# Kernel optimization log

Hardware: AMD Instinct MI355X
Metric: run time of the kernel (lower is better)

## Reference

```python
import jax, jax.numpy as jnp
import numpy as np

N_CLUSTERS = 2048
MAX_ITER = 5


def setup_inputs() -> dict:
    key = jax.random.key(0)
    k1, k2 = jax.random.split(key)
    X = jax.random.normal(k1, (131072, 128), dtype=jnp.float32)
    init_centroids = jax.random.normal(k2, (N_CLUSTERS, 128), dtype=jnp.float32)
    return {"X": X, "init_centroids": init_centroids}


def _euc_sim(a, b):
    # 2 a.b^T - |a|^2 - |b|^2  (negative squared euclidean distance)
    return (2.0 * (a @ b.T)
            - jnp.sum(a * a, axis=1)[:, None]
            - jnp.sum(b * b, axis=1)[None, :])


def reference(X, init_centroids):
    K = init_centroids.shape[0]

    def step(centroids, _):
        sim = _euc_sim(X, centroids)              # [N, K]
        closest = jnp.argmax(sim, axis=-1)         # [N]
        sums = jax.ops.segment_sum(X, closest, num_segments=K)        # [K, d]
        counts = jax.ops.segment_sum(jnp.ones_like(closest, dtype=X.dtype),
                                     closest, num_segments=K)         # [K]
        # full-batch branch: c_grad = mask @ x / mask.sum(-1), NaN -> 0
        c_grad = jnp.where(counts[:, None] > 0, sums / jnp.maximum(counts, 1.0)[:, None], 0.0)
        # minibatch is None => lr = 1 => centroids <- c_grad
        return c_grad, closest

    centroids, closest_hist = jax.lax.scan(step, init_centroids, None, length=MAX_ITER)
    labels = closest_hist[-1]
    return centroids, labels
```

## Files before the change

### kernel.cpp

```cpp
#include <hip/hip_runtime.h>
#include <hip/hip_bf16.h>

#define NP 131072
#define D 128
#define KC 2048
#define ITERS 5
#define CG 8

#define TAU 0.015f
#define CNOFF 49152

#if defined(__has_builtin)
#if __has_builtin(__builtin_amdgcn_global_load_lds)
#define USE_GLL 1
#endif
#endif

typedef short bf16x8 __attribute__((ext_vector_type(8)));
typedef float f32x4 __attribute__((ext_vector_type(4)));

__device__ inline unsigned short f2bf(float x) {
    __hip_bfloat16 b = __float2bfloat16(x);
    return *reinterpret_cast<unsigned short*>(&b);
}
__device__ inline float bf2f(unsigned short u) {
    union { unsigned int i; float f; } c; c.i = ((unsigned int)u) << 16; return c.f;
}

__device__ inline size_t pslot(int k, int d, int hl) {
    int g = k >> 4, t15 = k & 15, ks = d >> 5, q = (d >> 3) & 3, e = d & 7;
    return ((size_t)((ks * 128 + g) * 2 + hl)) * 512 + (q * 16 + t15) * 8 + e;
}

#if USE_GLL
#define GLL16(srcp, dstp) __builtin_amdgcn_global_load_lds( \
    (const __attribute__((address_space(1))) unsigned int*)(srcp), \
    (__attribute__((address_space(3))) unsigned int*)(dstp), 16, 0, 0)
#define GLL4(srcp, dstp) __builtin_amdgcn_global_load_lds( \
    (const __attribute__((address_space(1))) unsigned int*)(srcp), \
    (__attribute__((address_space(3))) unsigned int*)(dstp), 4, 0, 0)
#else
#define GLL16(srcp, dstp) do { *(uint4*)((char*)(dstp) + lane * 16) = *(const uint4*)(srcp); } while (0)
#define GLL4(srcp, dstp)  do { *(unsigned int*)((char*)(dstp) + lane * 4) = *(const unsigned int*)(srcp); } while (0)
#endif

__global__ void init_kernel(const float* __restrict__ initC,
                            double* __restrict__ C64, double* __restrict__ CT64,
                            unsigned short* __restrict__ Pn,
                            double* __restrict__ cn64, float* __restrict__ cn32,
                            int* __restrict__ counter) {
    __shared__ double sred[4];
    int tid = threadIdx.x;
    int t = blockIdx.x * 256 + tid;
    float v = initC[t];
    double dv = (double)v;
    C64[t] = dv;
    CT64[(size_t)(t & 127) * KC + (t >> 7)] = dv;
    unsigned short h = f2bf(v);
    int k = t >> 7, d = t & 127;
    Pn[pslot(k, d, 0)] = h;
    Pn[pslot(k, d, 1)] = f2bf(v - bf2f(h));
    double s = dv * dv;
#pragma unroll
    for (int m = 1; m < 64; m <<= 1) s += __shfl_xor(s, m, 64);
    if ((tid & 63) == 0) sred[tid >> 6] = s;
    __syncthreads();
    if (tid == 0)   { double ss = sred[0] + sred[1]; cn64[k] = ss; cn32[k] = (float)ss; }
    if (tid == 128) { double ss = sred[2] + sred[3]; cn64[k] = ss; cn32[k] = (float)ss; }
    if (blockIdx.x == 0 && tid == 0) *counter = 0;
}

__global__ __launch_bounds__(256, 3)
void assign_kernel(const float* __restrict__ X,
                   const unsigned short* __restrict__ Pn,
                   const float* __restrict__ cnorm,
                   int* __restrict__ labels,
                   int* __restrict__ list,
                   int* __restrict__ counter) {
    __shared__ __align__(16) char lds[49664];

    const int tid = threadIdx.x;
    const int lane = tid & 63;
    const int wid = tid >> 6;
    const int wrow = wid >> 1;
    const int wcol = wid & 1;
    const int t15 = lane & 15;
    const int q = lane >> 4;
    const int pbase = blockIdx.x * 64;
    const char* PnB = (const char*)Pn;

#pragma unroll
    for (int i = 0; i < 8; i++) {
        int f = i * 256 + tid;
        int row = f >> 5, c4 = f & 31;
        float4 v = *(const float4*)&X[(size_t)(pbase + row) * D + c4 * 4];
        unsigned short h0 = f2bf(v.x), h1 = f2bf(v.y), h2 = f2bf(v.z), h3 = f2bf(v.w);
        unsigned short l0 = f2bf(v.x - bf2f(h0)), l1 = f2bf(v.y - bf2f(h1));
        unsigned short l2 = f2bf(v.z - bf2f(h2)), l3 = f2bf(v.w - bf2f(h3));
        uint2 ph = { (unsigned)h0 | ((unsigned)h1 << 16), (unsigned)h2 | ((unsigned)h3 << 16) };
        uint2 pl = { (unsigned)l0 | ((unsigned)l1 << 16), (unsigned)l2 | ((unsigned)l3 << 16) };
        int ad = (row * 256 + c4 * 8) ^ ((row & 7) << 4);
        *(uint2*)(lds + ad) = ph;
        *(uint2*)(lds + 16384 + ad) = pl;
    }
    __syncthreads();

    bf16x8 rah[2][4], ral[2][4];
#pragma unroll
    for (int rt = 0; rt < 2; rt++) {
        int row = wrow * 32 + rt * 16 + t15;
        int sw = (row & 7) << 4;
#pragma unroll
        for (int ks = 0; ks < 4; ks++) {
            int ad = (row * 256 + ks * 64 + q * 16) ^ sw;
            rah[rt][ks] = *(const bf16x8*)(lds + ad);
            ral[rt][ks] = *(const bf16x8*)(lds + 16384 + ad);
        }
    }
    __syncthreads();

    float b1[8], b2[8];
    int i1[8];
#pragma unroll
    for (int s = 0; s < 8; s++) { b1[s] = -INFINITY; b2[s] = -INFINITY; i1[s] = 0x7fffffff; }

#pragma unroll
    for (int i = 0; i < 4; i++) {
        int seg = wid * 4 + i;
        GLL16(PnB + seg * 1024 + lane * 16, lds + seg * 1024);
    }
#pragma unroll
    for (int i = 0; i < 4; i++) {
        int seg = wid * 4 + i;
        GLL16(PnB + (size_t)(1 * 128) * 2048 + seg * 1024 + lane * 16,
              lds + 16384 + seg * 1024);
    }

#define STEP(KS, VMSTR) do {                                                  \
        asm volatile("s_waitcnt vmcnt(" VMSTR ")" ::: "memory");              \
        __builtin_amdgcn_s_barrier();                                         \
        asm volatile("" ::: "memory");                                        \
        __builtin_amdgcn_sched_barrier(0);                                    \
        int t_ = ct * 4 + (KS);                                               \
        int s2_ = t_ + 2;                                                     \
        int s2c_ = (s2_ > 63) ? 63 : s2_;                                     \
        char* bstage_ = lds + (unsigned)(s2_ % 3) * 16384;                    \
        const char* nsrc_ = PnB + ((size_t)((s2c_ & 3) * 128 + (s2c_ >> 2) * 8)) * 2048; \
        _Pragma("unroll")                                                     \
        for (int i_ = 0; i_ < 4; i_++) {                                      \
            int seg_ = wid * 4 + i_;                                          \
            GLL16(nsrc_ + seg_ * 1024 + lane * 16, bstage_ + seg_ * 1024);    \
        }                                                                     \
        if ((KS) == 0) {                                                      \
            const float* cs_ = cnorm + ct * 128;                              \
            GLL4(cs_ + lane, lds + CNOFF);                                    \
            GLL4(cs_ + 64 + lane, lds + CNOFF + 256);                         \
        }                                                                     \
        const char* bcur_ = lds + (unsigned)(t_ % 3) * 16384;                 \
        __builtin_amdgcn_s_setprio(1);                                        \
        _Pragma("unroll")                                                     \
        for (int cj_ = 0; cj_ < 4; cj_++) {                                   \
            int gl_ = wcol * 4 + cj_;                                         \
            bf16x8 bh_ = *(const bf16x8*)(bcur_ + gl_ * 2048 + lane * 16);    \
            bf16x8 bl_ = *(const bf16x8*)(bcur_ + gl_ * 2048 + 1024 + lane * 16); \
            _Pragma("unroll")                                                 \
            for (int rt_ = 0; rt_ < 2; rt_++) {                               \
                acc[rt_][cj_] = __builtin_amdgcn_mfma_f32_16x16x32_bf16(rah[rt_][KS], bh_, acc[rt_][cj_], 0, 0, 0); \
                acc[rt_][cj_] = __builtin_amdgcn_mfma_f32_16x16x32_bf16(rah[rt_][KS], bl_, acc[rt_][cj_], 0, 0, 0); \
                acc[rt_][cj_] = __builtin_amdgcn_mfma_f32_16x16x32_bf16(ral[rt_][KS], bh_, acc[rt_][cj_], 0, 0, 0); \
            }                                                                 \
        }                                                                     \
        __builtin_amdgcn_s_setprio(0);                                        \
    } while (0)

    for (int ct = 0; ct < KC / 128; ct++) {
        f32x4 acc[2][4];
#pragma unroll
        for (int rt = 0; rt < 2; rt++)
#pragma unroll
            for (int cj = 0; cj < 4; cj++) acc[rt][cj] = (f32x4){0.f, 0.f, 0.f, 0.f};

        STEP(0, "4");
        STEP(1, "6");
        STEP(2, "6");
        STEP(3, "4");

        const float* cnL = (const float*)(lds + CNOFF);
#pragma unroll
        for (int cj = 0; cj < 4; cj++) {
            int col = ct * 128 + wcol * 64 + cj * 16 + t15;
            float cnv = cnL[wcol * 64 + cj * 16 + t15];
#pragma unroll
            for (int rt = 0; rt < 2; rt++)
#pragma unroll
                for (int rg = 0; rg < 4; rg++) {
                    int s = rt * 4 + rg;
                    float sv = __builtin_fmaf(2.0f, acc[rt][cj][rg], -cnv);
                    float nb2 = __builtin_amdgcn_fmed3f(b1[s], b2[s], sv);
                    bool gt1 = sv > b1[s];
                    i1[s] = gt1 ? col : i1[s];
                    b1[s] = fmaxf(b1[s], sv);
                    b2[s] = nb2;
                }
        }
    }
#undef STEP

#pragma unroll
    for (int s = 0; s < 8; s++) {
#pragma unroll
        for (int m = 1; m < 16; m <<= 1) {
            float ob1 = __shfl_xor(b1[s], m, 64);
            int   oi  = __shfl_xor(i1[s], m, 64);
            float ob2 = __shfl_xor(b2[s], m, 64);
            bool gt = ob1 > b1[s];
            bool eq = ob1 == b1[s];
            float nb2 = gt ? fmaxf(b1[s], ob2) : fmaxf(b2[s], ob1);
            nb2 = eq ? b1[s] : nb2;
            int ni = gt ? oi : i1[s];
            ni = (eq && oi < i1[s]) ? oi : ni;
            b1[s] = gt ? ob1 : b1[s];
            b2[s] = nb2;
            i1[s] = ni;
        }
    }

    __syncthreads();
    float* mb1 = (float*)lds;
    float* mb2 = ((float*)lds) + 128;
    int*   mi1 = (int*)(((float*)lds) + 256);
    if (t15 == 0) {
#pragma unroll
        for (int rt = 0; rt < 2; rt++)
#pragma unroll
            for (int rg = 0; rg < 4; rg++) {
                int s = rt * 4 + rg;
                int row = wrow * 32 + rt * 16 + q * 4 + rg;
                mb1[wcol * 64 + row] = b1[s];
                mb2[wcol * 64 + row] = b2[s];
                mi1[wcol * 64 + row] = i1[s];
            }
    }
    __syncthreads();
    if (tid < 64) {
        float a1 = mb1[tid], a2 = mb2[tid];  int ai = mi1[tid];
        float c1 = mb1[64 + tid], c2 = mb2[64 + tid];  int ci = mi1[64 + tid];
        float best, second;  int bi;
        if (a1 > c1)      { best = a1; bi = ai; second = fmaxf(a2, c1); }
        else if (a1 < c1) { best = c1; bi = ci; second = fmaxf(c2, a1); }
        else              { best = a1; bi = (ai < ci) ? ai : ci; second = a1; }
        int p = pbase + tid;
        labels[p] = bi;
        if (best - second < TAU) {
            int idx = atomicAdd(counter, 1);
            list[idx] = p;
        }
    }
}

__global__ void recheck_kernel(const float* __restrict__ X,
                               const double* __restrict__ CT64,
                               const double* __restrict__ cn64,
                               const int* __restrict__ list,
                               const int* __restrict__ counter,
                               int* __restrict__ labels) {
    __shared__ float xrow[D];
    __shared__ double rb[4];
    __shared__ int ri[4];
    int cnt = *counter;
    for (int ii = blockIdx.x; ii < cnt; ii += gridDim.x) {
        int p = list[ii];
        __syncthreads();
        if (threadIdx.x < D) xrow[threadIdx.x] = X[(size_t)p * D + threadIdx.x];
        __syncthreads();
        double xn = 0.0;
#pragma unroll 16
        for (int d = 0; d < D; d++) {
            double xv = (double)xrow[d];
            xn = fma(xv, xv, xn);
        }
        double best = -1.0e300;
        int bi = 0x7fffffff;
#pragma unroll
        for (int g = 0; g < 8; g++) {
            int c = threadIdx.x + 256 * g;
            double acc = 0.0;
#pragma unroll 16
            for (int d = 0; d < D; d++)
                acc = fma((double)xrow[d], CT64[(size_t)d * KC + c], acc);
            double s = 2.0 * acc - xn - cn64[c];
            if (s > best || (s == best && c < bi)) { best = s; bi = c; }
        }
#pragma unroll
        for (int m = 1; m < 64; m <<= 1) {
            double ob = __shfl_xor(best, m, 64);
            int oi = __shfl_xor(bi, m, 64);
            if (ob > best || (ob == best && oi < bi)) { best = ob; bi = oi; }
        }
        int w = threadIdx.x >> 6;
        if ((threadIdx.x & 63) == 0) { rb[w] = best; ri[w] = bi; }
        __syncthreads();
        if (threadIdx.x == 0) {
            double bb = rb[0]; int bbi = ri[0];
            for (int w2 = 1; w2 < 4; w2++)
                if (rb[w2] > bb || (rb[w2] == bb && ri[w2] < bbi)) { bb = rb[w2]; bbi = ri[w2]; }
            labels[p] = bbi;
        }
    }
}

__global__ __launch_bounds__(512)
void accum_kernel(const float* __restrict__ X,
                  const int* __restrict__ labels,
                  double* __restrict__ C64, double* __restrict__ CT64,
                  unsigned short* __restrict__ Pn,
                  double* __restrict__ cn64, float* __restrict__ cn32,
                  int* __restrict__ counter,
                  float* __restrict__ outC) {
    __shared__ double sred[8][CG][64][2];
    __shared__ int cred[8][CG];
    __shared__ int cntS[CG];
    __shared__ double cnp[2][8];
    const int lane = threadIdx.x & 63;
    const int w = threadIdx.x >> 6;
    const int kbase = blockIdx.x * CG;
    const int base0 = w * (NP / 8);
    double s0[CG], s1[CG];
    int cnt[CG];
#pragma unroll
    for (int c = 0; c < CG; c++) { s0[c] = 0.0; s1[c] = 0.0; cnt[c] = 0; }

    for (int it = 0; it < (NP / 8) / 256; it++) {
        int4 lab = *(const int4*)&labels[base0 + it * 256 + lane * 4];
#pragma unroll
        for (int j = 0; j < 4; j++) {
            int lv = (j == 0) ? lab.x : (j == 1) ? lab.y : (j == 2) ? lab.z : lab.w;
            int rel = lv - kbase;
#pragma unroll
            for (int c = 0; c < CG; c++) {
                unsigned long long m = __ballot(rel == c);
                cnt[c] += __popcll(m);
                while (m) {
                    int b = __ffsll(m) - 1;
                    m &= m - 1;
                    int p = base0 + it * 256 + b * 4 + j;
                    float2 v = *(const float2*)&X[(size_t)p * D + lane * 2];
                    s0[c] += (double)v.x;
                    s1[c] += (double)v.y;
                }
            }
        }
    }
#pragma unroll
    for (int c = 0; c < CG; c++) {
        sred[w][c][lane][0] = s0[c];
        sred[w][c][lane][1] = s1[c];
    }
    if (lane < CG) cred[w][lane] = cnt[lane];
    __syncthreads();

    if (threadIdx.x < CG) {
        int s = 0;
#pragma unroll
        for (int ww = 0; ww < 8; ww++) s += cred[ww][threadIdx.x];
        cntS[threadIdx.x] = s;
    }
    __syncthreads();

#pragma unroll
    for (int rep = 0; rep < 2; rep++) {
        int idx = rep * 512 + threadIdx.x;
        int c = idx >> 7, d = idx & 127;
        double s = 0.0;
#pragma unroll
        for (int ww = 0; ww < 8; ww++) s += sred[ww][c][d >> 1][d & 1];
        int k = kbase + c;
        int n = cntS[c];
        double v = (n > 0) ? s / (double)n : 0.0;
        C64[(size_t)k * D + d] = v;
        CT64[(size_t)d * KC + k] = v;
        float vf = (float)v;
        unsigned short h = f2bf(vf);
        Pn[pslot(k, d, 0)] = h;
        Pn[pslot(k, d, 1)] = f2bf(vf - bf2f(h));
        if (outC) outC[(size_t)k * D + d] = vf;
        double sq = v * v;
#pragma unroll
        for (int m = 1; m < 64; m <<= 1) sq += __shfl_xor(sq, m, 64);
        if (lane == 0) cnp[rep][w] = sq;
    }
    __syncthreads();
    if (threadIdx.x < CG) {
        int c = threadIdx.x;
        int rep = c >> 2, wp = (c & 3) * 2;
        double cn = cnp[rep][wp] + cnp[rep][wp + 1];
        cn64[kbase + c] = cn;
        cn32[kbase + c] = (float)cn;
    }
    if (blockIdx.x == 0 && threadIdx.x == 0) *counter = 0;
}

__global__ void lab2f_kernel(const int* __restrict__ labels, float* __restrict__ out) {
    int t = blockIdx.x * 256 + threadIdx.x;
    out[t] = (float)labels[t];
}

extern "C" void kernel_launch(void* const* d_in, const int* in_sizes, int n_in,
                              void* d_out, int out_size, void* d_ws, size_t ws_size,
                              hipStream_t stream) {
    const float* X = (const float*)d_in[0];
    const float* initC = (const float*)d_in[1];
    float* out = (float*)d_out;

    char* w = (char*)d_ws;
    const size_t MB = 1u << 20;
    double* C64    = (double*)(w);
    double* CT64   = (double*)(w + 4 * MB);
    unsigned short* Pn = (unsigned short*)(w + 6 * MB);
    int*    labels = (int*)   (w + 7 * MB);
    int*    list   = (int*)   (w + 7 * MB + 512 * 1024);
    double* cn64   = (double*)(w + 8 * MB);
    float*  cn32   = (float*) (w + 8 * MB + 16 * 1024);
    int*    counter= (int*)   (w + 8 * MB + 32 * 1024);

    init_kernel<<<(KC * D) / 256, 256, 0, stream>>>(initC, C64, CT64, Pn, cn64, cn32, counter);

    for (int it = 0; it < ITERS; it++) {
        assign_kernel<<<NP / 64, 256, 0, stream>>>(X, Pn, cn32, labels, list, counter);
        recheck_kernel<<<2048, 256, 0, stream>>>(X, CT64, cn64, list, counter, labels);
        accum_kernel<<<KC / CG, 512, 0, stream>>>(X, labels, C64, CT64, Pn, cn64, cn32,
                                                  counter, (it == ITERS - 1) ? out : nullptr);
    }
    lab2f_kernel<<<NP / 256, 256, 0, stream>>>(labels, out + (size_t)KC * D);
}
```

Baseline: 1.832 ms.

## Switch assign kernel from 16x16x32 to 32x32x16 MFMA tiles

Replaces the 16x16x32 bf16 MFMA tiles in the assignment GEMM with 32x32x16 tiles. This changes the packed centroid layout (pslot), how A fragments are loaded, and the accumulator shape. The argmax/second-best reduction is reworked for the 32-lane column layout. The aim is fewer MFMA issues and B-fragment LDS reads per output. In exchange it takes more accumulator registers and per-row tracking state (16 rows per lane) and one extra shuffle step in the reduction.

```diff
diff --git a/kernel.cpp b/kernel.cpp
--- a/kernel.cpp
+++ b/kernel.cpp
@@ -17,7 +17,7 @@
 #endif
 
 typedef short bf16x8 __attribute__((ext_vector_type(8)));
-typedef float f32x4 __attribute__((ext_vector_type(4)));
+typedef float f32x16 __attribute__((ext_vector_type(16)));
 
 __device__ inline unsigned short f2bf(float x) {
     __hip_bfloat16 b = __float2bfloat16(x);
@@ -28,8 +28,11 @@
 }
 
 __device__ inline size_t pslot(int k, int d, int hl) {
-    int g = k >> 4, t15 = k & 15, ks = d >> 5, q = (d >> 3) & 3, e = d & 7;
-    return ((size_t)((ks * 128 + g) * 2 + hl)) * 512 + (q * 16 + t15) * 8 + e;
+    int ct = k >> 7, kc = k & 127, g2 = kc >> 5, c32 = kc & 31;
+    int ks32 = d >> 5, sub = (d >> 4) & 1, kk = d & 15;
+    int lane = (kk >> 3) * 32 + c32, e = kk & 7;
+    int f = sub * 8 + g2 * 2 + hl;
+    return ((size_t)(ks32 * 128 + ct * 8)) * 1024 + f * 512 + lane * 8 + e;
 }
 
 #if USE_GLL
@@ -84,8 +87,8 @@
     const int wid = tid >> 6;
     const int wrow = wid >> 1;
     const int wcol = wid & 1;
-    const int t15 = lane & 15;
-    const int q = lane >> 4;
+    const int l31 = lane & 31;
+    const int lh = lane >> 5;
     const int pbase = blockIdx.x * 64;
     const char* PnB = (const char*)Pn;
 
@@ -105,24 +108,23 @@
     }
     __syncthreads();
 
-    bf16x8 rah[2][4], ral[2][4];
-#pragma unroll
-    for (int rt = 0; rt < 2; rt++) {
-        int row = wrow * 32 + rt * 16 + t15;
+    bf16x8 rah[8], ral[8];
+    {
+        int row = wrow * 32 + l31;
         int sw = (row & 7) << 4;
 #pragma unroll
-        for (int ks = 0; ks < 4; ks++) {
-            int ad = (row * 256 + ks * 64 + q * 16) ^ sw;
-            rah[rt][ks] = *(const bf16x8*)(lds + ad);
-            ral[rt][ks] = *(const bf16x8*)(lds + 16384 + ad);
-        }
-    }
-    __syncthreads();
-
-    float b1[8], b2[8];
-    int i1[8];
-#pragma unroll
-    for (int s = 0; s < 8; s++) { b1[s] = -INFINITY; b2[s] = -INFINITY; i1[s] = 0x7fffffff; }
+        for (int ks16 = 0; ks16 < 8; ks16++) {
+            int ad = (row * 256 + ks16 * 32 + lh * 16) ^ sw;
+            rah[ks16] = *(const bf16x8*)(lds + ad);
+            ral[ks16] = *(const bf16x8*)(lds + 16384 + ad);
+        }
+    }
+    __syncthreads();
+
+    float b1[16], b2[16];
+    int i1[16];
+#pragma unroll
+    for (int s = 0; s < 16; s++) { b1[s] = -INFINITY; b2[s] = -INFINITY; i1[s] = 0x7fffffff; }
 
 #pragma unroll
     for (int i = 0; i < 4; i++) {
@@ -159,26 +161,26 @@
         const char* bcur_ = lds + (unsigned)(t_ % 3) * 16384;                 \
         __builtin_amdgcn_s_setprio(1);                                        \
         _Pragma("unroll")                                                     \
-        for (int cj_ = 0; cj_ < 4; cj_++) {                                   \
-            int gl_ = wcol * 4 + cj_;                                         \
-            bf16x8 bh_ = *(const bf16x8*)(bcur_ + gl_ * 2048 + lane * 16);    \
-            bf16x8 bl_ = *(const bf16x8*)(bcur_ + gl_ * 2048 + 1024 + lane * 16); \
+        for (int sub_ = 0; sub_ < 2; sub_++) {                                \
             _Pragma("unroll")                                                 \
-            for (int rt_ = 0; rt_ < 2; rt_++) {                               \
-                acc[rt_][cj_] = __builtin_amdgcn_mfma_f32_16x16x32_bf16(rah[rt_][KS], bh_, acc[rt_][cj_], 0, 0, 0); \
-                acc[rt_][cj_] = __builtin_amdgcn_mfma_f32_16x16x32_bf16(rah[rt_][KS], bl_, acc[rt_][cj_], 0, 0, 0); \
-                acc[rt_][cj_] = __builtin_amdgcn_mfma_f32_16x16x32_bf16(ral[rt_][KS], bh_, acc[rt_][cj_], 0, 0, 0); \
+            for (int cj_ = 0; cj_ < 2; cj_++) {                               \
+                int f_ = sub_ * 8 + (wcol * 2 + cj_) * 2;                     \
+                bf16x8 bh_ = *(const bf16x8*)(bcur_ + f_ * 1024 + lane * 16); \
+                bf16x8 bl_ = *(const bf16x8*)(bcur_ + f_ * 1024 + 1024 + lane * 16); \
+                acc32[cj_] = __builtin_amdgcn_mfma_f32_32x32x16_bf16(rah[(KS) * 2 + sub_], bh_, acc32[cj_], 0, 0, 0); \
+                acc32[cj_] = __builtin_amdgcn_mfma_f32_32x32x16_bf16(rah[(KS) * 2 + sub_], bl_, acc32[cj_], 0, 0, 0); \
+                acc32[cj_] = __builtin_amdgcn_mfma_f32_32x32x16_bf16(ral[(KS) * 2 + sub_], bh_, acc32[cj_], 0, 0, 0); \
             }                                                                 \
         }                                                                     \
         __builtin_amdgcn_s_setprio(0);                                        \
     } while (0)
 
     for (int ct = 0; ct < KC / 128; ct++) {
-        f32x4 acc[2][4];
-#pragma unroll
-        for (int rt = 0; rt < 2; rt++)
-#pragma unroll
-            for (int cj = 0; cj < 4; cj++) acc[rt][cj] = (f32x4){0.f, 0.f, 0.f, 0.f};
+        f32x16 acc32[2];
+#pragma unroll
+        for (int cj = 0; cj < 2; cj++)
+#pragma unroll
+            for (int r = 0; r < 16; r++) acc32[cj][r] = 0.f;
 
         STEP(0, "4");
         STEP(1, "6");
@@ -187,29 +189,26 @@
 
         const float* cnL = (const float*)(lds + CNOFF);
 #pragma unroll
-        for (int cj = 0; cj < 4; cj++) {
-            int col = ct * 128 + wcol * 64 + cj * 16 + t15;
-            float cnv = cnL[wcol * 64 + cj * 16 + t15];
-#pragma unroll
-            for (int rt = 0; rt < 2; rt++)
-#pragma unroll
-                for (int rg = 0; rg < 4; rg++) {
-                    int s = rt * 4 + rg;
-                    float sv = __builtin_fmaf(2.0f, acc[rt][cj][rg], -cnv);
-                    float nb2 = __builtin_amdgcn_fmed3f(b1[s], b2[s], sv);
-                    bool gt1 = sv > b1[s];
-                    i1[s] = gt1 ? col : i1[s];
-                    b1[s] = fmaxf(b1[s], sv);
-                    b2[s] = nb2;
-                }
+        for (int cj = 0; cj < 2; cj++) {
+            int col = ct * 128 + wcol * 64 + cj * 32 + l31;
+            float cnv = cnL[wcol * 64 + cj * 32 + l31];
+#pragma unroll
+            for (int r = 0; r < 16; r++) {
+                float sv = __builtin_fmaf(2.0f, acc32[cj][r], -cnv);
+                float nb2 = __builtin_amdgcn_fmed3f(b1[r], b2[r], sv);
+                bool gt1 = sv > b1[r];
+                i1[r] = gt1 ? col : i1[r];
+                b1[r] = fmaxf(b1[r], sv);
+                b2[r] = nb2;
+            }
         }
     }
 #undef STEP
 
 #pragma unroll
-    for (int s = 0; s < 8; s++) {
-#pragma unroll
-        for (int m = 1; m < 16; m <<= 1) {
+    for (int s = 0; s < 16; s++) {
+#pragma unroll
+        for (int m = 1; m < 32; m <<= 1) {
             float ob1 = __shfl_xor(b1[s], m, 64);
             int   oi  = __shfl_xor(i1[s], m, 64);
             float ob2 = __shfl_xor(b2[s], m, 64);
@@ -229,17 +228,14 @@
     float* mb1 = (float*)lds;
     float* mb2 = ((float*)lds) + 128;
     int*   mi1 = (int*)(((float*)lds) + 256);
-    if (t15 == 0) {
-#pragma unroll
-        for (int rt = 0; rt < 2; rt++)
-#pragma unroll
-            for (int rg = 0; rg < 4; rg++) {
-                int s = rt * 4 + rg;
-                int row = wrow * 32 + rt * 16 + q * 4 + rg;
-                mb1[wcol * 64 + row] = b1[s];
-                mb2[wcol * 64 + row] = b2[s];
-                mi1[wcol * 64 + row] = i1[s];
-            }
+    if (l31 == 0) {
+#pragma unroll
+        for (int r = 0; r < 16; r++) {
+            int row = wrow * 32 + (r & 3) + 8 * (r >> 2) + 4 * lh;
+            mb1[wcol * 64 + row] = b1[r];
+            mb2[wcol * 64 + row] = b2[r];
+            mi1[wcol * 64 + row] = i1[r];
+        }
     }
     __syncthreads();
     if (tid < 64) {
```

New measurement: 2.059 ms. 1.12x slower.
